# Optimization experiments

Hardware: AMD Instinct MI355X
Metric: run time of the kernel (lower is better)

## Reference

```python
import jax, jax.numpy as jnp
import numpy as np
from jax import lax

B, T, SDIM, ADIM, HDIM, NH, NBLK, MAXT = 4, 512, 64, 32, 512, 8, 6, 4096
DFF = 4 * HDIM
S = 3 * T  # (num_state_tokens + 1) * context_len
DH = HDIM // NH


def _layernorm(x, g, b, eps=1e-5):
    m = jnp.mean(x, axis=-1, keepdims=True)
    v = jnp.mean((x - m) ** 2, axis=-1, keepdims=True)
    return (x - m) * lax.rsqrt(v + eps) * g + b


def setup_inputs() -> dict:
    key = jax.random.key(0)
    ks = iter(jax.random.split(key, 40))

    def nrm(shape, scale=0.02):
        return jax.random.normal(next(ks), shape, jnp.float32) * scale

    inp = {
        "timesteps": jax.random.randint(next(ks), (B, T), 0, MAXT),
        "state_0": jax.random.normal(next(ks), (B, T, SDIM), jnp.float32),
        "state_1": jax.random.normal(next(ks), (B, T, SDIM), jnp.float32),
        "actions": jax.random.normal(next(ks), (B, T, ADIM), jnp.float32),
        # embeddings / input projections
        "time_emb": nrm((MAXT, HDIM)),
        "Ws": nrm((SDIM, HDIM)), "bs": jnp.zeros((HDIM,), jnp.float32),
        "Wa": nrm((ADIM, HDIM)), "ba": jnp.zeros((HDIM,), jnp.float32),
        # stacked per-block transformer params (leading axis = n_blocks)
        "Wq": nrm((NBLK, HDIM, HDIM)), "bq": jnp.zeros((NBLK, HDIM), jnp.float32),
        "Wk": nrm((NBLK, HDIM, HDIM)), "bk": jnp.zeros((NBLK, HDIM), jnp.float32),
        "Wv": nrm((NBLK, HDIM, HDIM)), "bv": jnp.zeros((NBLK, HDIM), jnp.float32),
        "Wo": nrm((NBLK, HDIM, HDIM)), "bo": jnp.zeros((NBLK, HDIM), jnp.float32),
        "W1": nrm((NBLK, HDIM, DFF)), "b1": jnp.zeros((NBLK, DFF), jnp.float32),
        "W2": nrm((NBLK, DFF, HDIM)), "b2": jnp.zeros((NBLK, HDIM), jnp.float32),
        "ln1_g": jnp.ones((NBLK, HDIM), jnp.float32), "ln1_b": jnp.zeros((NBLK, HDIM), jnp.float32),
        "ln2_g": jnp.ones((NBLK, HDIM), jnp.float32), "ln2_b": jnp.zeros((NBLK, HDIM), jnp.float32),
        # embed layernorm + action head
        "eln_g": jnp.ones((HDIM,), jnp.float32), "eln_b": jnp.zeros((HDIM,), jnp.float32),
        "Wp": nrm((HDIM, ADIM)), "bp": jnp.zeros((ADIM,), jnp.float32),
    }
    return inp


def reference(timesteps, state_0, state_1, actions, time_emb, Ws, bs, Wa, ba,
              Wq, bq, Wk, bk, Wv, bv, Wo, bo, W1, b1, W2, b2,
              ln1_g, ln1_b, ln2_g, ln2_b, eln_g, eln_b, Wp, bp):
    te = time_emb[timesteps]                       # (B, T, H)
    s0 = state_0 @ Ws + bs + te                    # shared state embedding
    s1 = state_1 @ Ws + bs + te
    ae = actions @ Wa + ba + te
    # interleave: (B, T, 3, H) -> (B, 3T, H), token order [s0, s1, a] per timestep
    h = jnp.stack([s0, s1, ae], axis=2).reshape(B, S, HDIM)
    h = _layernorm(h, eln_g, eln_b)

    causal = jnp.tril(jnp.ones((S, S), dtype=bool))
    scale = 1.0 / float(DH) ** 0.5

    def block(x, p):
        wq, bq_, wk, bk_, wv, bv_, wo, bo_, w1, b1_, w2, b2_, g1, be1, g2, be2 = p
        q = (x @ wq + bq_).reshape(B, S, NH, DH)
        k = (x @ wk + bk_).reshape(B, S, NH, DH)
        v = (x @ wv + bv_).reshape(B, S, NH, DH)
        scores = jnp.einsum('bihd,bjhd->bhij', q, k) * scale
        scores = jnp.where(causal, scores, -jnp.inf)
        attn = jax.nn.softmax(scores, axis=-1)
        ctx = jnp.einsum('bhij,bjhd->bihd', attn, v).reshape(B, S, HDIM)
        x = x + (ctx @ wo + bo_)
        x = _layernorm(x, g1, be1)
        mlp = jax.nn.gelu(x @ w1 + b1_, approximate=False) @ w2 + b2_
        x = _layernorm(x + mlp, g2, be2)
        return x, None

    h, _ = lax.scan(block, h,
                    (Wq, bq, Wk, bk, Wv, bv, Wo, bo, W1, b1, W2, b2,
                     ln1_g, ln1_b, ln2_g, ln2_b))

    h = h.reshape(B, T, 3, HDIM)                   # (B, T, num_tokens, H)
    act_in = h[:, :, 1]                            # token index -2 = last state token
    return act_in @ Wp + bp                        # (B, T, act_dim)
```

## Files before the change

kernel.cpp:

```cpp
#include <hip/hip_runtime.h>
#include <hip/hip_bf16.h>
#include <math.h>

#define BB 4
#define TT 512
#define SDIM 64
#define ADIM 32
#define HDIM 512
#define NH 8
#define NBLK 6
#define DFF 2048
#define SS 1536
#define DH 64
#define MS (BB*SS)

typedef __attribute__((ext_vector_type(8))) __bf16 bf16x8;
typedef __attribute__((ext_vector_type(4))) float f32x4;

__device__ __forceinline__ __bf16 f2b(float x) { return (__bf16)x; }

__device__ __forceinline__ void gll16(const void* g, void* l) {
    __builtin_amdgcn_global_load_lds(
        (const __attribute__((address_space(1))) unsigned int*)g,
        (__attribute__((address_space(3))) unsigned int*)l, 16, 0, 0);
}

__global__ __launch_bounds__(512) void embed_ln_kernel(
    const int* __restrict__ timesteps,
    const float* __restrict__ state0, const float* __restrict__ state1,
    const float* __restrict__ actions, const float* __restrict__ time_emb,
    const float* __restrict__ Ws, const float* __restrict__ bs,
    const float* __restrict__ Wa, const float* __restrict__ ba,
    const float* __restrict__ eg, const float* __restrict__ eb,
    __bf16* __restrict__ h_bf)
{
    __shared__ float xs[8][64];
    __shared__ float acc_s[8][512];
    __shared__ int tss[8];
    int c = blockIdx.x, t = blockIdx.y, b = blockIdx.z;
    int i0 = c * 8;
    int tid = threadIdx.x;
    int K = (t == 2) ? ADIM : SDIM;
    int ksh = (t == 2) ? 5 : 6;
    const float* W    = (t == 2) ? Wa : Ws;
    const float* bias = (t == 2) ? ba : bs;
    const float* src  = (t == 0) ? state0  + ((size_t)(b*TT + i0)) * SDIM
                      : (t == 1) ? state1  + ((size_t)(b*TT + i0)) * SDIM
                                 : actions + ((size_t)(b*TT + i0)) * ADIM;

    if (tid < 8) tss[tid] = timesteps[b*TT + i0 + tid];
    for (int idx = tid; idx < 8 * K; idx += 512) {
        int r = idx >> ksh, kk = idx & (K - 1);
        xs[r][kk] = src[r * K + kk];
    }
    __syncthreads();

    float acc[8];
    #pragma unroll
    for (int r = 0; r < 8; ++r)
        acc[r] = bias[tid] + time_emb[(size_t)tss[r] * HDIM + tid];
    for (int kk = 0; kk < K; ++kk) {
        float w = W[(size_t)kk * HDIM + tid];
        #pragma unroll
        for (int r = 0; r < 8; ++r) acc[r] += xs[r][kk] * w;
    }
    #pragma unroll
    for (int r = 0; r < 8; ++r) acc_s[r][tid] = acc[r];
    __syncthreads();

    int w = tid >> 6, lane = tid & 63;
    float4 p0 = *(const float4*)&acc_s[w][lane * 8];
    float4 p1 = *(const float4*)&acc_s[w][lane * 8 + 4];
    float v[8] = {p0.x, p0.y, p0.z, p0.w, p1.x, p1.y, p1.z, p1.w};
    float s = 0.f, sq = 0.f;
    #pragma unroll
    for (int u = 0; u < 8; ++u) { s += v[u]; sq += v[u] * v[u]; }
    #pragma unroll
    for (int off = 1; off < 64; off <<= 1) { s += __shfl_xor(s, off); sq += __shfl_xor(sq, off); }
    float mean = s * (1.f / HDIM);
    float var  = sq * (1.f / HDIM) - mean * mean;
    float inv  = rsqrtf(var + 1e-5f);
    float4 g0 = *(const float4*)(eg + lane * 8), g1 = *(const float4*)(eg + lane * 8 + 4);
    float4 b0 = *(const float4*)(eb + lane * 8), b1 = *(const float4*)(eb + lane * 8 + 4);
    float gg[8] = {g0.x, g0.y, g0.z, g0.w, g1.x, g1.y, g1.z, g1.w};
    float bbv[8] = {b0.x, b0.y, b0.z, b0.w, b1.x, b1.y, b1.z, b1.w};
    __bf16 o8[8];
    #pragma unroll
    for (int u = 0; u < 8; ++u) o8[u] = f2b((v[u] - mean) * inv * gg[u] + bbv[u]);
    int row = b * SS + (i0 + w) * 3 + t;
    *(uint4*)(h_bf + (size_t)row * HDIM + lane * 8) = *(uint4*)o8;
}

template<bool TWO>
__global__ __launch_bounds__(256) void ln_add_kernel(
    __bf16* __restrict__ h_bf, const __bf16* __restrict__ ya,
    const __bf16* __restrict__ yb,
    const float* __restrict__ g, const float* __restrict__ bvec)
{
    int w = threadIdx.x >> 6, lane = threadIdx.x & 63;
    int row = blockIdx.x * 4 + w;
    size_t base = (size_t)row * HDIM + lane * 8;
    bf16x8 h8 = *(const bf16x8*)(h_bf + base);
    bf16x8 a8 = *(const bf16x8*)(ya + base);
    bf16x8 b8;
    if (TWO) b8 = *(const bf16x8*)(yb + base);
    float v[8], s = 0.f, sq = 0.f;
    #pragma unroll
    for (int u = 0; u < 8; ++u) {
        v[u] = (float)h8[u] + (float)a8[u] + (TWO ? (float)b8[u] : 0.f);
        s += v[u]; sq += v[u] * v[u];
    }
    #pragma unroll
    for (int off = 1; off < 64; off <<= 1) { s += __shfl_xor(s, off); sq += __shfl_xor(sq, off); }
    float mean = s * (1.f / HDIM);
    float var  = sq * (1.f / HDIM) - mean * mean;
    float inv  = rsqrtf(var + 1e-5f);
    float4 g0 = *(const float4*)(g + lane * 8), g1 = *(const float4*)(g + lane * 8 + 4);
    float4 b0 = *(const float4*)(bvec + lane * 8), b1 = *(const float4*)(bvec + lane * 8 + 4);
    float gg[8] = {g0.x, g0.y, g0.z, g0.w, g1.x, g1.y, g1.z, g1.w};
    float bbv[8] = {b0.x, b0.y, b0.z, b0.w, b1.x, b1.y, b1.z, b1.w};
    __bf16 o8[8];
    #pragma unroll
    for (int u = 0; u < 8; ++u) o8[u] = f2b((v[u] - mean) * inv * gg[u] + bbv[u]);
    *(uint4*)(h_bf + base) = *(uint4*)o8;
}

__global__ __launch_bounds__(256) void pack_kernel(
    const float* __restrict__ Wq, const float* __restrict__ Wk,
    const float* __restrict__ Wv, const float* __restrict__ Wo,
    const float* __restrict__ W1, const float* __restrict__ W2,
    const float* __restrict__ bq_, const float* __restrict__ bk_, const float* __restrict__ bv_,
    __bf16* __restrict__ wqkvT, __bf16* __restrict__ woT,
    __bf16* __restrict__ w1T, __bf16* __restrict__ w2T, float* __restrict__ biasq)
{
    int lyr = blockIdx.y;
    const float* wq = Wq + (size_t)lyr * HDIM * HDIM;
    const float* wk = Wk + (size_t)lyr * HDIM * HDIM;
    const float* wv = Wv + (size_t)lyr * HDIM * HDIM;
    const float* wo = Wo + (size_t)lyr * HDIM * HDIM;
    const float* w1 = W1 + (size_t)lyr * HDIM * DFF;
    const float* w2 = W2 + (size_t)lyr * DFF * HDIM;
    const float* bqL = bq_ + (size_t)lyr * HDIM;
    const float* bkL = bk_ + (size_t)lyr * HDIM;
    const float* bvL = bv_ + (size_t)lyr * HDIM;
    wqkvT += (size_t)lyr * 1536 * 512;
    woT   += (size_t)lyr * 512 * 512;
    w1T   += (size_t)lyr * 2048 * 512;
    w2T   += (size_t)lyr * 512 * 2048;
    biasq += (size_t)lyr * 1536;

    int bid = blockIdx.x;
    int tid = threadIdx.x;
    if (bid == 768) {
        for (int i = tid; i < 1536; i += 256)
            biasq[i] = (i < 512) ? bqL[i] : ((i < 1024) ? bkL[i-512] : bvL[i-1024]);
        return;
    }
    __shared__ float Ls[64][65];
    const float* src; __bf16* dst; int K, N, kt, nt;
    if (bid < 192) {
        int sec = bid / 64, t = bid % 64;
        src = (sec == 0) ? wq : (sec == 1) ? wk : wv;
        dst = wqkvT + (size_t)sec * 512 * 512;
        K = 512; N = 512; nt = t >> 3; kt = t & 7;
    } else if (bid < 256) {
        int t = bid - 192; src = wo; dst = woT; K = 512; N = 512; nt = t >> 3; kt = t & 7;
    } else if (bid < 512) {
        int t = bid - 256; src = w1; dst = w1T; K = 512; N = 2048; nt = t >> 3; kt = t & 7;
    } else {
        int t = bid - 512; src = w2; dst = w2T; K = 2048; N = 512; nt = t & 7; kt = t >> 3;
    }
    int k0 = kt * 64, n0 = nt * 64;
    int rr = tid >> 4, cc = (tid & 15) * 4;
    #pragma unroll
    for (int p = 0; p < 4; ++p) {
        float4 v = *(const float4*)(src + (size_t)(k0 + rr + p*16) * N + n0 + cc);
        Ls[rr + p*16][cc] = v.x; Ls[rr + p*16][cc+1] = v.y;
        Ls[rr + p*16][cc+2] = v.z; Ls[rr + p*16][cc+3] = v.w;
    }
    __syncthreads();
    int nn = tid >> 3, kc = (tid & 7) * 8;
    #pragma unroll
    for (int p = 0; p < 2; ++p) {
        __bf16 t8[8];
        #pragma unroll
        for (int t2 = 0; t2 < 8; ++t2) t8[t2] = f2b(Ls[kc + t2][nn + p*32]);
        *(uint4*)(dst + (size_t)(n0 + nn + p*32) * K + k0 + kc) = *(uint4*)t8;
    }
}

template<int MT, bool VTMODE>
__global__ __launch_bounds__(256) void gemm_mfma(
    const __bf16* __restrict__ A, const __bf16* __restrict__ Bt,
    const float* __restrict__ bias, __bf16* __restrict__ C,
    __bf16* __restrict__ VTout,
    int N, int Ksub, int lda, int ldb, int ldc, int gelu, size_t cSplitStride)
{
    constexpr int MI = MT / 32;
    constexpr int SMB = 2*MT*64 + 2*128*64;
    __shared__ __align__(16) char sm[SMB];
    __bf16* As = (__bf16*)sm;
    __bf16* Bs = (__bf16*)(sm + 2*MT*64);
    int tid = threadIdx.x;
    int wave = tid >> 6, lane = tid & 63;
    int l15 = lane & 15, quad = lane >> 4;
    int wy = wave >> 1, wx = wave & 1;
    int m0 = blockIdx.y * MT, n0 = blockIdx.x * 128;
    int zs = blockIdx.z;
    int kbase = zs * Ksub;
    C += (size_t)zs * cSplitStride;

    int srow = lane >> 2;
    int clog = (lane & 3) ^ ((lane >> 3) & 3);
    int pchunk = (quad ^ ((l15 >> 1) & 3)) * 8;

    f32x4 acc[MI][4];
    #pragma unroll
    for (int i = 0; i < MI; ++i)
        #pragma unroll
        for (int j = 0; j < 4; ++j) acc[i][j] = (f32x4){0.f,0.f,0.f,0.f};

    const __bf16* Abase = A  + (size_t)m0 * lda + kbase + clog * 8;
    const __bf16* Bbase = Bt + (size_t)n0 * ldb + kbase + clog * 8;
    int NK = Ksub >> 5;

    #pragma unroll
    for (int q = 0; q < MT/64; ++q) {
        int r0 = (wave * (MT/64) + q) * 16;
        gll16(Abase + (size_t)(r0 + srow) * lda, As + r0*32);
    }
    #pragma unroll
    for (int q = 0; q < 2; ++q) {
        int r0 = (wave * 2 + q) * 16;
        gll16(Bbase + (size_t)(r0 + srow) * ldb, Bs + r0*32);
    }

    for (int kt = 0; kt < NK; ++kt) {
        int buf = kt & 1;
        __syncthreads();
        if (kt + 1 < NK) {
            int k0 = (kt + 1) << 5;
            #pragma unroll
            for (int q = 0; q < MT/64; ++q) {
                int r0 = (wave * (MT/64) + q) * 16;
                gll16(Abase + (size_t)(r0 + srow) * lda + k0, As + ((buf^1)*MT + r0)*32);
            }
            #pragma unroll
            for (int q = 0; q < 2; ++q) {
                int r0 = (wave * 2 + q) * 16;
                gll16(Bbase + (size_t)(r0 + srow) * ldb + k0, Bs + ((buf^1)*128 + r0)*32);
            }
        }
        bf16x8 af[MI], bf[4];
        #pragma unroll
        for (int i = 0; i < MI; ++i)
            af[i] = *(const bf16x8*)&As[(buf*MT + wy*(MT/2) + i*16 + l15)*32 + pchunk];
        #pragma unroll
        for (int j = 0; j < 4; ++j)
            bf[j] = *(const bf16x8*)&Bs[(buf*128 + wx*64 + j*16 + l15)*32 + pchunk];
        #pragma unroll
        for (int i = 0; i < MI; ++i)
            #pragma unroll
            for (int j = 0; j < 4; ++j)
                acc[i][j] = __builtin_amdgcn_mfma_f32_16x16x32_bf16(af[i], bf[j], acc[i][j], 0, 0, 0);
    }

    if (VTMODE && n0 >= 1024) {
        __syncthreads();
        __bf16* T = (__bf16*)sm;
        #pragma unroll
        for (int j = 0; j < 4; ++j) {
            int dl = wx*64 + j*16 + l15;
            float bv = bias[n0 + dl];
            int x31 = dl & 31;
            #pragma unroll
            for (int i = 0; i < MI; ++i) {
                int sc = wy*16 + i*4 + quad;
                int phys = sc ^ x31;
                __bf16 v4[4];
                #pragma unroll
                for (int r = 0; r < 4; ++r) v4[r] = f2b(acc[i][j][r] + bv);
                *(uint2*)(T + dl*128 + phys*4) = *(uint2*)v4;
            }
        }
        __syncthreads();
        int dl = tid >> 1, sh = (tid & 1) * 64;
        int dglob = n0 - 1024 + dl;
        int bb = m0 / SS, srel = m0 - bb*SS;
        __bf16* vb = VTout + ((size_t)(bb*NH + (dglob >> 6)) * 64 + (dglob & 63)) * SS + srel + sh;
        int x31 = dl & 31;
        #pragma unroll
        for (int u = 0; u < 8; ++u) {
            int c0 = (sh >> 2) + u*2;
            uint2 lo = *(const uint2*)(T + dl*128 + ((c0    ) ^ x31)*4);
            uint2 hi = *(const uint2*)(T + dl*128 + ((c0 + 1) ^ x31)*4);
            uint4 o; o.x = lo.x; o.y = lo.y; o.z = hi.x; o.w = hi.y;
            *(uint4*)(vb + u*8) = o;
        }
        return;
    }

    #pragma unroll
    for (int j = 0; j < 4; ++j) {
        int cc = n0 + wx*64 + j*16 + l15;
        float bv = (zs == 0) ? bias[cc] : 0.f;
        #pragma unroll
        for (int i = 0; i < MI; ++i) {
            #pragma unroll
            for (int r = 0; r < 4; ++r) {
                int rr = m0 + wy*(MT/2) + i*16 + quad*4 + r;
                float v = acc[i][j][r] + bv;
                if (gelu) {
                    float u2 = v * (0.7978845608f + 0.0356774081f * v * v);
                    float e  = __builtin_amdgcn_exp2f(u2 * 2.885390082f);
                    v = v * (1.f - __builtin_amdgcn_rcpf(e + 1.f));
                }
                C[(size_t)rr * ldc + cc] = f2b(v);
            }
        }
    }
}

#define SM_C 0.18033688011112042f

__device__ __forceinline__ unsigned pack2bf(float a, float b)
{
    union { __bf16 h[2]; unsigned u; } t;
    t.h[0] = (__bf16)a; t.h[1] = (__bf16)b;
    return t.u;
}

__device__ __forceinline__ bf16x8 ptrans(const float* p0, const float* p1, int lane)
{
    int l15 = lane & 15, quad = lane >> 4;
    unsigned pk0a = pack2bf(p0[0], p0[1]), pk0b = pack2bf(p0[2], p0[3]);
    unsigned pk1a = pack2bf(p1[0], p1[1]), pk1b = pack2bf(p1[2], p1[3]);
    int sA = l15 + (quad & 1) * 32;
    int sB = sA + 16;
    int hi = quad >> 1;
    unsigned a0A = (unsigned)__shfl((int)pk0a, sA);
    unsigned a1A = (unsigned)__shfl((int)pk1a, sA);
    unsigned b0A = (unsigned)__shfl((int)pk0b, sA);
    unsigned b1A = (unsigned)__shfl((int)pk1b, sA);
    unsigned a0B = (unsigned)__shfl((int)pk0a, sB);
    unsigned a1B = (unsigned)__shfl((int)pk1a, sB);
    unsigned b0B = (unsigned)__shfl((int)pk0b, sB);
    unsigned b1B = (unsigned)__shfl((int)pk1b, sB);
    union { unsigned u[4]; bf16x8 v; } pb;
    pb.u[0] = hi ? a1A : a0A;
    pb.u[1] = hi ? b1A : b0A;
    pb.u[2] = hi ? a1B : a0B;
    pb.u[3] = hi ? b1B : b0B;
    return pb.v;
}

__global__ __launch_bounds__(256, 3) void attn_kernel(
    __bf16* qkc, const __bf16* __restrict__ VT)
{
    __shared__ __align__(16) char smem[32768];

    int x = blockIdx.x;
    int region = x >> 8;
    int j = x & 255;
    int i = j >> 5;
    int hb = j & 31;
    int qt = (region == 0) ? (23 - i) : (region == 1) ? (8 + i) : i;
    int h = hb >> 2, b = hb & 3;

    int tid = threadIdx.x;
    int w = tid >> 6, lane = tid & 63;
    int l15 = lane & 15, quad = lane >> 4;
    int qrow0 = qt * 64 + w * 16;

    const __bf16* qp = qkc + (size_t)(b*SS + qrow0 + l15) * 1024 + h*64 + quad*8;
    bf16x8 qf0 = *(const bf16x8*)qp;
    bf16x8 qf1 = *(const bf16x8*)(qp + 32);

    const __bf16* kgbase = qkc + (size_t)(b*SS) * 1024 + 512 + h*64;
    const __bf16* vgbase = VT + (size_t)(b*NH + h) * 64 * SS;
    int srow8 = lane >> 3;
    int clog  = (lane & 7) ^ ((lane >> 3) & 7);
    int sw0 = ((0*4 + quad) ^ (l15 & 7)) * 8;
    int sw1 = ((1*4 + quad) ^ (l15 & 7)) * 8;

    f32x4 o0 = {0.f,0.f,0.f,0.f}, o1 = o0, o2 = o0, o3 = o0;
    float sm_m = -1e30f, sm_l = 0.f;

    int nkt = qt + 1;

    #pragma unroll
    for (int q = 0; q < 2; ++q) {
        int r0 = (w*2 + q) * 8;
        gll16(kgbase + (size_t)(r0 + srow8) * 1024 + clog*8, (__bf16*)smem + r0*64);
        gll16(vgbase + (size_t)(r0 + srow8) * SS   + clog*8, (__bf16*)(smem + 16384) + r0*64);
    }
    __syncthreads();

    for (int jt = 0; jt < nkt; ++jt) {
        int buf = jt & 1;
        const __bf16* Kb = (const __bf16*)(smem + buf * 8192);
        const __bf16* Vb = (const __bf16*)(smem + 16384 + buf * 8192);
        if (jt + 1 < nkt) {
            int kb2 = (jt + 1) * 64;
            __bf16* Kn = (__bf16*)(smem + (buf ^ 1) * 8192);
            __bf16* Vn = (__bf16*)(smem + 16384 + (buf ^ 1) * 8192);
            #pragma unroll
            for (int q = 0; q < 2; ++q) {
                int r0 = (w*2 + q) * 8;
                gll16(kgbase + (size_t)(kb2 + r0 + srow8) * 1024 + clog*8, Kn + r0*64);
                gll16(vgbase + (size_t)(r0 + srow8) * SS + kb2 + clog*8,   Vn + r0*64);
            }
        }
        int kb = jt * 64;

        f32x4 s[4];
        __builtin_amdgcn_s_setprio(1);
        #pragma unroll
        for (int f = 0; f < 4; ++f) {
            bf16x8 k0 = *(const bf16x8*)(Kb + (16*f + l15)*64 + sw0);
            bf16x8 k1 = *(const bf16x8*)(Kb + (16*f + l15)*64 + sw1);
            f32x4 sf = {0.f,0.f,0.f,0.f};
            sf = __builtin_amdgcn_mfma_f32_16x16x32_bf16(k0, qf0, sf, 0, 0, 0);
            sf = __builtin_amdgcn_mfma_f32_16x16x32_bf16(k1, qf1, sf, 0, 0, 0);
            s[f] = sf;
        }
        __builtin_amdgcn_s_setprio(0);

        if (kb + 63 > qrow0) {
            int qrow = qrow0 + l15;
            #pragma unroll
            for (int f = 0; f < 4; ++f)
                #pragma unroll
                for (int r = 0; r < 4; ++r)
                    if (kb + 16*f + quad*4 + r > qrow) s[f][r] = -1e30f;
        }

        float tm = -1e30f;
        #pragma unroll
        for (int f = 0; f < 4; ++f)
            #pragma unroll
            for (int r = 0; r < 4; ++r) tm = fmaxf(tm, s[f][r]);
        tm = fmaxf(tm, __shfl_xor(tm, 16));
        tm = fmaxf(tm, __shfl_xor(tm, 32));

        if (!__all(tm <= sm_m + 64.f)) {
            float mnew = fmaxf(sm_m, tm);
            float alpha = __builtin_amdgcn_exp2f((sm_m - mnew) * SM_C);
            sm_l *= alpha;
            o0 *= alpha; o1 *= alpha; o2 *= alpha; o3 *= alpha;
            sm_m = mnew;
        }

        float pp[4][4];
        float rs = 0.f;
        #pragma unroll
        for (int f = 0; f < 4; ++f)
            #pragma unroll
            for (int r = 0; r < 4; ++r) {
                float pv = __builtin_amdgcn_exp2f((s[f][r] - sm_m) * SM_C);
                pp[f][r] = pv;
                rs += pv;
            }
        rs += __shfl_xor(rs, 16);
        rs += __shfl_xor(rs, 32);
        sm_l += rs;

        bf16x8 pb01 = ptrans(pp[0], pp[1], lane);
        bf16x8 pb23 = ptrans(pp[2], pp[3], lane);

        __builtin_amdgcn_s_setprio(1);
        #pragma unroll
        for (int ii = 0; ii < 4; ++ii) {
            bf16x8 va = *(const bf16x8*)(Vb + (16*ii + l15)*64 + sw0);
            bf16x8 vb = *(const bf16x8*)(Vb + (16*ii + l15)*64 + sw1);
            f32x4* op = (ii == 0) ? &o0 : (ii == 1) ? &o1 : (ii == 2) ? &o2 : &o3;
            *op = __builtin_amdgcn_mfma_f32_16x16x32_bf16(va, pb01, *op, 0, 0, 0);
            *op = __builtin_amdgcn_mfma_f32_16x16x32_bf16(vb, pb23, *op, 0, 0, 0);
        }
        __builtin_amdgcn_s_setprio(0);
        __syncthreads();
    }

    float* otw = (float*)smem + w * 16 * 68;
    float inv = 1.f / sm_l;
    #pragma unroll
    for (int r = 0; r < 4; ++r) {
        otw[l15*68 +  0 + quad*4 + r] = o0[r] * inv;
        otw[l15*68 + 16 + quad*4 + r] = o1[r] * inv;
        otw[l15*68 + 32 + quad*4 + r] = o2[r] * inv;
        otw[l15*68 + 48 + quad*4 + r] = o3[r] * inv;
    }
    asm volatile("s_waitcnt lgkmcnt(0)" ::: "memory");
    int row = lane >> 2, ch = (lane & 3) * 16;
    union { __bf16 hh[16]; uint4 q4[2]; } ob;
    #pragma unroll
    for (int t2 = 0; t2 < 16; ++t2) ob.hh[t2] = f2b(otw[row*68 + ch + t2]);
    __bf16* cp = qkc + (size_t)(b*SS + qrow0 + row) * 1024 + h*64 + ch;
    *(uint4*)cp = ob.q4[0];
    *(uint4*)(cp + 8) = ob.q4[1];
}

__global__ __launch_bounds__(256) void proj_kernel(
    const __bf16* __restrict__ h_bf, const float* __restrict__ Wp,
    const float* __restrict__ bp, float* __restrict__ out)
{
    int rid = blockIdx.x * 8 + (threadIdx.x >> 5);
    int col = threadIdx.x & 31;
    int b = rid / TT, i = rid - b * TT;
    const __bf16* x = h_bf + ((size_t)(b*SS) + 3*i + 1) * HDIM;
    float acc = bp[col];
    for (int k8 = 0; k8 < HDIM/8; ++k8) {
        bf16x8 x8 = *(const bf16x8*)(x + k8*8);
        #pragma unroll
        for (int u = 0; u < 8; ++u)
            acc += (float)x8[u] * Wp[(k8*8 + u) * ADIM + col];
    }
    out[(size_t)rid * ADIM + col] = acc;
}

extern "C" void kernel_launch(void* const* d_in, const int* in_sizes, int n_in,
                              void* d_out, int out_size, void* d_ws, size_t ws_size,
                              hipStream_t stream)
{
    (void)in_sizes; (void)n_in; (void)out_size; (void)ws_size;
    const int*   timesteps = (const int*)  d_in[0];
    const float* state0    = (const float*)d_in[1];
    const float* state1    = (const float*)d_in[2];
    const float* actions   = (const float*)d_in[3];
    const float* time_emb  = (const float*)d_in[4];
    const float* Ws  = (const float*)d_in[5];
    const float* bs  = (const float*)d_in[6];
    const float* Wa  = (const float*)d_in[7];
    const float* ba  = (const float*)d_in[8];
    const float* Wq  = (const float*)d_in[9];
    const float* bq  = (const float*)d_in[10];
    const float* Wk  = (const float*)d_in[11];
    const float* bk  = (const float*)d_in[12];
    const float* Wv  = (const float*)d_in[13];
    const float* bv  = (const float*)d_in[14];
    const float* Wo  = (const float*)d_in[15];
    const float* bo  = (const float*)d_in[16];
    const float* W1  = (const float*)d_in[17];
    const float* b1  = (const float*)d_in[18];
    const float* W2  = (const float*)d_in[19];
    const float* b2  = (const float*)d_in[20];
    const float* ln1g = (const float*)d_in[21];
    const float* ln1b = (const float*)d_in[22];
    const float* ln2g = (const float*)d_in[23];
    const float* ln2b = (const float*)d_in[24];
    const float* elng = (const float*)d_in[25];
    const float* elnb = (const float*)d_in[26];
    const float* Wp   = (const float*)d_in[27];
    const float* bp   = (const float*)d_in[28];
    float* out = (float*)d_out;

    const size_t SZ = (size_t)MS * HDIM;
    char* p = (char*)d_ws;
    __bf16* h_bf = (__bf16*)p;           p += SZ * 2;
    __bf16* qk   = (__bf16*)p;           p += (size_t)MS * 1024 * 2;
    __bf16* VT   = (__bf16*)p;           p += SZ * 2;
                      p += SZ * 2;
    __bf16* tmpA = (__bf16*)p;           p += SZ * 2;
    __bf16* tmpB = (__bf16*)p;           p += SZ * 2;
    __bf16* wqkvT = (__bf16*)p;          p += (size_t)NBLK * 1536 * 512 * 2;
    __bf16* woT   = (__bf16*)p;          p += (size_t)NBLK * 512 * 512 * 2;
    __bf16* w1T   = (__bf16*)p;          p += (size_t)NBLK * 2048 * 512 * 2;
    __bf16* w2T   = (__bf16*)p;          p += (size_t)NBLK * 512 * 2048 * 2;
    float*  biasq = (float*)p;           p += (size_t)NBLK * 1536 * 4;
    __bf16* hid   = qk;

    embed_ln_kernel<<<dim3(TT/8, 3, BB), 512, 0, stream>>>(timesteps, state0, state1, actions,
                                                           time_emb, Ws, bs, Wa, ba, elng, elnb, h_bf);

    pack_kernel<<<dim3(769, NBLK), 256, 0, stream>>>(Wq, Wk, Wv, Wo, W1, W2, bq, bk, bv,
                                                     wqkvT, woT, w1T, w2T, biasq);

    dim3 gQKV(1536/128, MS/128, 1);
    dim3 gWO (512/128,  MS/128, 1);
    dim3 gW2 (512/128,  MS/64, 2);
    dim3 gF1 (2048/128, MS/128, 1);

    for (int lyr = 0; lyr < NBLK; ++lyr) {
        const __bf16* wqkvT_l = wqkvT + (size_t)lyr * 1536 * 512;
        const __bf16* woT_l   = woT   + (size_t)lyr * 512 * 512;
        const __bf16* w1T_l   = w1T   + (size_t)lyr * 2048 * 512;
        const __bf16* w2T_l   = w2T   + (size_t)lyr * 512 * 2048;
        const float*  biasq_l = biasq + (size_t)lyr * 1536;

        gemm_mfma<128, true><<<gQKV, 256, 0, stream>>>(h_bf, wqkvT_l, biasq_l, qk, VT,
                                                       1536, 512, 512, 512, 1024, 0, 0);
        attn_kernel<<<dim3(768), 256, 0, stream>>>(qk, VT);
        gemm_mfma<128, false><<<gWO, 256, 0, stream>>>(qk, woT_l, bo + lyr*HDIM, tmpA, nullptr,
                                                       512, 512, 1024, 512, 512, 0, 0);
        ln_add_kernel<false><<<MS/4, 256, 0, stream>>>(h_bf, tmpA, nullptr,
                                                       ln1g + lyr*HDIM, ln1b + lyr*HDIM);
        gemm_mfma<128, false><<<gF1, 256, 0, stream>>>(h_bf, w1T_l, b1 + lyr*DFF, hid, nullptr,
                                                       2048, 512, 512, 512, 2048, 1, 0);
        gemm_mfma<64, false><<<gW2, 256, 0, stream>>>(hid, w2T_l, b2 + lyr*HDIM, tmpA, nullptr,
                                                      512, 1024, 2048, 2048, 512, 0, SZ);
        ln_add_kernel<true><<<MS/4, 256, 0, stream>>>(h_bf, tmpA, tmpB,
                                                      ln2g + lyr*HDIM, ln2b + lyr*HDIM);
    }

    proj_kernel<<<(BB*TT)/8, 256, 0, stream>>>(h_bf, Wp, bp, out);
}
```

Measured before the change: 953.9 us.

## Split-K the Wo projection and tidy attention softmax reductions

The attention-output projection now uses the 64-row tile GEMM with a two-way split-K along z, the same as the W2 GEMM. Its partial sums go to tmpA and tmpB and are summed in the LayerNorm-add kernel, which raises block count for the small-N GEMM. In the attention kernel the s_setprio hints are removed, the max and sum reductions become tree-shaped, and the exp argument becomes a single FMA with a hoisted -m*C term. Split-K adds an extra partial buffer write and read in exchange for more parallelism.

New measurement: 944.6 us. Within noise of the previous version (-1.0%).

```diff
diff --git a/kernel.cpp b/kernel.cpp
--- a/kernel.cpp
+++ b/kernel.cpp
@@ -414,7 +414,6 @@
         int kb = jt * 64;
 
         f32x4 s[4];
-        __builtin_amdgcn_s_setprio(1);
         #pragma unroll
         for (int f = 0; f < 4; ++f) {
             bf16x8 k0 = *(const bf16x8*)(Kb + (16*f + l15)*64 + sw0);
@@ -424,7 +423,6 @@
             sf = __builtin_amdgcn_mfma_f32_16x16x32_bf16(k1, qf1, sf, 0, 0, 0);
             s[f] = sf;
         }
-        __builtin_amdgcn_s_setprio(0);
 
         if (kb + 63 > qrow0) {
             int qrow = qrow0 + l15;
@@ -435,11 +433,11 @@
                     if (kb + 16*f + quad*4 + r > qrow) s[f][r] = -1e30f;
         }
 
-        float tm = -1e30f;
+        float tf[4];
         #pragma unroll
         for (int f = 0; f < 4; ++f)
-            #pragma unroll
-            for (int r = 0; r < 4; ++r) tm = fmaxf(tm, s[f][r]);
+            tf[f] = fmaxf(fmaxf(s[f][0], s[f][1]), fmaxf(s[f][2], s[f][3]));
+        float tm = fmaxf(fmaxf(tf[0], tf[1]), fmaxf(tf[2], tf[3]));
         tm = fmaxf(tm, __shfl_xor(tm, 16));
         tm = fmaxf(tm, __shfl_xor(tm, 32));
 
@@ -451,16 +449,17 @@
             sm_m = mnew;
         }
 
+        float negmC = -sm_m * SM_C;
         float pp[4][4];
-        float rs = 0.f;
-        #pragma unroll
-        for (int f = 0; f < 4; ++f)
-            #pragma unroll
-            for (int r = 0; r < 4; ++r) {
-                float pv = __builtin_amdgcn_exp2f((s[f][r] - sm_m) * SM_C);
-                pp[f][r] = pv;
-                rs += pv;
-            }
+        float rf[4];
+        #pragma unroll
+        for (int f = 0; f < 4; ++f) {
+            #pragma unroll
+            for (int r = 0; r < 4; ++r)
+                pp[f][r] = __builtin_amdgcn_exp2f(fmaf(s[f][r], SM_C, negmC));
+            rf[f] = (pp[f][0] + pp[f][1]) + (pp[f][2] + pp[f][3]);
+        }
+        float rs = (rf[0] + rf[1]) + (rf[2] + rf[3]);
         rs += __shfl_xor(rs, 16);
         rs += __shfl_xor(rs, 32);
         sm_l += rs;
@@ -468,7 +467,6 @@
         bf16x8 pb01 = ptrans(pp[0], pp[1], lane);
         bf16x8 pb23 = ptrans(pp[2], pp[3], lane);
 
-        __builtin_amdgcn_s_setprio(1);
         #pragma unroll
         for (int ii = 0; ii < 4; ++ii) {
             bf16x8 va = *(const bf16x8*)(Vb + (16*ii + l15)*64 + sw0);
@@ -477,7 +475,6 @@
             *op = __builtin_amdgcn_mfma_f32_16x16x32_bf16(va, pb01, *op, 0, 0, 0);
             *op = __builtin_amdgcn_mfma_f32_16x16x32_bf16(vb, pb23, *op, 0, 0, 0);
         }
-        __builtin_amdgcn_s_setprio(0);
         __syncthreads();
     }
 
@@ -576,8 +573,7 @@
                                                      wqkvT, woT, w1T, w2T, biasq);
 
     dim3 gQKV(1536/128, MS/128, 1);
-    dim3 gWO (512/128,  MS/128, 1);
-    dim3 gW2 (512/128,  MS/64, 2);
+    dim3 gO  (512/128,  MS/64, 2);
     dim3 gF1 (2048/128, MS/128, 1);
 
     for (int lyr = 0; lyr < NBLK; ++lyr) {
@@ -590,14 +586,14 @@
         gemm_mfma<128, true><<<gQKV, 256, 0, stream>>>(h_bf, wqkvT_l, biasq_l, qk, VT,
                                                        1536, 512, 512, 512, 1024, 0, 0);
         attn_kernel<<<dim3(768), 256, 0, stream>>>(qk, VT);
-        gemm_mfma<128, false><<<gWO, 256, 0, stream>>>(qk, woT_l, bo + lyr*HDIM, tmpA, nullptr,
-                                                       512, 512, 1024, 512, 512, 0, 0);
-        ln_add_kernel<false><<<MS/4, 256, 0, stream>>>(h_bf, tmpA, nullptr,
-                                                       ln1g + lyr*HDIM, ln1b + lyr*HDIM);
+        gemm_mfma<64, false><<<gO, 256, 0, stream>>>(qk, woT_l, bo + lyr*HDIM, tmpA, nullptr,
+                                                     512, 256, 1024, 512, 512, 0, SZ);
+        ln_add_kernel<true><<<MS/4, 256, 0, stream>>>(h_bf, tmpA, tmpB,
+                                                      ln1g + lyr*HDIM, ln1b + lyr*HDIM);
         gemm_mfma<128, false><<<gF1, 256, 0, stream>>>(h_bf, w1T_l, b1 + lyr*DFF, hid, nullptr,
                                                        2048, 512, 512, 512, 2048, 1, 0);
-        gemm_mfma<64, false><<<gW2, 256, 0, stream>>>(hid, w2T_l, b2 + lyr*HDIM, tmpA, nullptr,
-                                                      512, 1024, 2048, 2048, 512, 0, SZ);
+        gemm_mfma<64, false><<<gO, 256, 0, stream>>>(hid, w2T_l, b2 + lyr*HDIM, tmpA, nullptr,
+                                                     512, 1024, 2048, 2048, 512, 0, SZ);
         ln_add_kernel<true><<<MS/4, 256, 0, stream>>>(h_bf, tmpA, tmpB,
                                                       ln2g + lyr*HDIM, ln2b + lyr*HDIM);
     }
```
